# Kernel optimization log

Measured on AMD Instinct MI355X. Metric: run time of the kernel, lower is better.

The kernel has to match this reference:

```python
import jax, jax.numpy as jnp
import numpy as np

B, C, N, M = 4, 192, 160, 160
HEADS, DH = 4, 32
HID = HEADS * DH
NMEM = 4
SCALE = DH ** -0.5


def setup_inputs() -> dict:
    key = jax.random.key(0)
    ks = jax.random.split(key, 8)
    std = 0.05
    return {
        "x": jax.random.normal(ks[0], (B, C, N, M), jnp.float32),
        "gq": jnp.ones((C,), jnp.float32),
        "gk": jnp.ones((C,), jnp.float32),
        "gv": jnp.ones((C,), jnp.float32),
        "Wq": jax.random.normal(ks[1], (HID, C), jnp.float32) * std,
        "Wk": jax.random.normal(ks[2], (HID, C), jnp.float32) * std,
        "Wv": jax.random.normal(ks[3], (HID, C), jnp.float32) * std,
        "mem_kv": jax.random.normal(ks[4], (2, HEADS, NMEM, DH), jnp.float32),
        "Wo": jax.random.normal(ks[5], (C, HID), jnp.float32) * std,
        "bo": jnp.zeros((C,), jnp.float32),
        "Wr": jax.random.normal(ks[6], (C, 2 * C), jnp.float32) * std,
    }


def _rms(x, g):
    # lucidrains RMSNorm over channel axis 1: F.normalize(x, dim=1) * g * sqrt(dim)
    n = jnp.sqrt(jnp.sum(x * x, axis=1, keepdims=True))
    gshape = (1, -1) + (1,) * (x.ndim - 2)
    return x / jnp.maximum(n, 1e-12) * g.reshape(gshape) * jnp.sqrt(jnp.asarray(x.shape[1], x.dtype))


def _axial_attn(q_ft, k_ft, v_map, rep, Wq, Wk, Wv, mem_kv, Wo, bo, gq, gk, gv):
    # q_ft: (b, c, Lq) compact queries (spatial (1,Lq) in the original)
    # k_ft: (b, c, Lk) compact keys; original repeats them `rep` times -> (Lk*rep) keys
    # v_map: (b, c, Lk, rep) values (full map, not broadcast)
    # Exact math of softmax over [NMEM + Lk*rep] keys, exploiting the rep-fold
    # duplicated key scores so attn(key i, copy j) has identical weight p_i:
    #   out = sum_mem p_j mem_v_j + sum_i p_i * (sum_rep v[i, r])
    b = q_ft.shape[0]
    q = jnp.einsum('hdc,bcq->bhqd', Wq.reshape(HEADS, DH, -1), _rms(q_ft, gq))
    k = jnp.einsum('hdc,bck->bhkd', Wk.reshape(HEADS, DH, -1), _rms(k_ft, gk))
    v = jnp.einsum('hdc,bckr->bhkrd', Wv.reshape(HEADS, DH, -1), _rms(v_map, gv))
    v_sum = v.sum(axis=3)  # (b,h,Lk,d)
    mem_k, mem_v = mem_kv[0], mem_kv[1]
    s_k = jnp.einsum('bhqd,bhkd->bhqk', q, k) * SCALE      # (b,h,Lq,Lk)
    s_m = jnp.einsum('bhqd,hjd->bhqj', q, mem_k) * SCALE   # (b,h,Lq,NMEM)
    mx = jnp.maximum(s_k.max(-1), s_m.max(-1))             # (b,h,Lq)
    e_k = jnp.exp(s_k - mx[..., None])
    e_m = jnp.exp(s_m - mx[..., None])
    Z = e_m.sum(-1) + rep * e_k.sum(-1)                    # rep copies of each key
    out = (jnp.einsum('bhqj,hjd->bhqd', e_m, mem_v)
           + jnp.einsum('bhqk,bhkd->bhqd', e_k, v_sum)) / Z[..., None]
    out = out.transpose(0, 2, 1, 3).reshape(b, -1, HID)    # (b,Lq,hid), (h d) channel order
    return jnp.einsum('ck,bqk->bcq', Wo, out) + bo[None, :, None]  # (b,c,Lq)


def reference(x, gq, gk, gv, Wq, Wk, Wv, mem_kv, Wo, bo, Wr):
    # x: (b,c,n,m); mask=None path
    row_ft = x.mean(axis=3)  # (b,c,n)
    col_ft = x.mean(axis=2)  # (b,c,m)
    # row attention: n queries, keys = col_ft repeated n times, values = x^T (spatial (m,n))
    row_attn = _axial_attn(row_ft, col_ft, x.transpose(0, 1, 3, 2), N,
                           Wq, Wk, Wv, mem_kv, Wo, bo, gq, gk, gv)  # (b,c,n)
    # col attention (shared weights): m queries, keys = row_ft repeated m times, values = x
    col_attn = _axial_attn(col_ft, row_ft, x, M,
                           Wq, Wk, Wv, mem_kv, Wo, bo, gq, gk, gv)  # (b,c,m)
    # broadcast to (b,c,n,m), concat on channels, 1x1 conv reduce (bias=False)
    Wr1, Wr2 = Wr[:, :C], Wr[:, C:]
    out = (jnp.einsum('dc,bcn->bdn', Wr1, row_attn)[:, :, :, None]
           + jnp.einsum('dc,bcm->bdm', Wr2, col_attn)[:, :, None, :])
    return out
```

## Files before the change

kernel.cpp:

```cpp
#include <hip/hip_runtime.h>
#include <math.h>

constexpr int B_ = 4, C_ = 192, N_ = 160, M_ = 160;
constexpr int NM_ = N_ * M_;
constexpr float SQRT_C = 13.856406460551018f;
constexpr float SCALE_ = 0.17677669529663687f;

__device__ __forceinline__ float wred_sum(float v) {
    #pragma unroll
    for (int o = 32; o > 0; o >>= 1) v += __shfl_xor(v, o, 64);
    return v;
}
__device__ __forceinline__ float wred_max(float v) {
    #pragma unroll
    for (int o = 32; o > 0; o >>= 1) v = fmaxf(v, __shfl_xor(v, o, 64));
    return v;
}

__global__ void prep_kernel(const float* __restrict__ Wr, const float* __restrict__ Wo,
                            const float* __restrict__ bo,
                            const float* __restrict__ Wq, const float* __restrict__ Wk,
                            const float* __restrict__ Wv, const float* __restrict__ gq,
                            const float* __restrict__ gk, const float* __restrict__ gv,
                            float* __restrict__ WfT, float* __restrict__ bfb,
                            float* __restrict__ WT) {
    int bx = blockIdx.x, tid = threadIdx.x;
    if (bx < 192) {
        int sub = tid >> 7, hd = tid & 127;
        int pair = bx * 2 + sub;
        int t = pair / 192, dch = pair % 192;
        const float* wr = Wr + dch * 384 + t * 192;
        float acc = 0.f;
        for (int c = 0; c < 192; c++) acc += wr[c] * Wo[c * 128 + hd];
        WfT[hd * 384 + pair] = acc;
        if (hd == 0) {
            float s = 0.f;
            for (int c = 0; c < 192; c++) s += wr[c] * bo[c];
            bfb[pair] = s;
        }
    } else {
        int g = (bx - 192) * 256 + tid;
        int mat = g / 24576, r2 = g % 24576;
        int c = r2 >> 7, hd = r2 & 127;
        const float* W = (mat == 0) ? Wq : ((mat == 1) ? Wk : Wv);
        const float* gv_ = (mat == 0) ? gq : ((mat == 1) ? gk : gv);
        WT[g] = gv_[c] * W[hd * 192 + c];
    }
}

__global__ void ssq_part_kernel(const float* __restrict__ x, float* __restrict__ psum) {
    int bx = blockIdx.x;
    int chunk = bx / 400, blk = bx % 400;
    int g = blk * 256 + threadIdx.x;
    int b = g / NM_, nm = g - b * NM_;
    const float* xp = x + ((size_t)(b * C_ + chunk * 32)) * NM_ + nm;
    float ssq = 0.f;
    #pragma unroll
    for (int cc = 0; cc < 32; cc++) { float v = xp[(size_t)cc * NM_]; ssq += v * v; }
    psum[chunk * (B_ * NM_) + g] = ssq;
}

__global__ void rnorm_kernel(const float* __restrict__ psum, float* __restrict__ rn) {
    int g = blockIdx.x * 256 + threadIdx.x;
    float s = 0.f;
    #pragma unroll
    for (int ch = 0; ch < 6; ch++) s += psum[ch * (B_ * NM_) + g];
    rn[g] = SQRT_C / fmaxf(sqrtf(s), 1e-12f);
}

__global__ void rowcol_kernel(const float* __restrict__ x, const float* __restrict__ rn,
                              float* __restrict__ rowft, float* __restrict__ colft,
                              float* __restrict__ Srow, float* __restrict__ Scol) {
    __shared__ float cpart[8][2][160];
    int bc = blockIdx.x;
    int b = bc / C_;
    int tid = threadIdx.x, w = tid >> 6, lane = tid & 63;
    const float* xp = x + (size_t)bc * NM_;
    const float* rp = rn + (size_t)b * NM_;
    int m0 = lane, m1 = lane + 64, m2 = lane + 128;
    bool ok2 = (m2 < M_);
    float cr0 = 0, cr1 = 0, cr2 = 0, cn0 = 0, cn1 = 0, cn2 = 0;
    for (int n = w; n < N_; n += 8) {
        const float* xr = xp + n * M_;
        const float* rr = rp + n * M_;
        float a0 = xr[m0], a1 = xr[m1], a2 = ok2 ? xr[m2] : 0.f;
        float r0 = rr[m0], r1 = rr[m1], r2 = ok2 ? rr[m2] : 0.f;
        float b0 = a0 * r0, b1 = a1 * r1, b2 = a2 * r2;
        cr0 += a0; cr1 += a1; cr2 += a2;
        cn0 += b0; cn1 += b1; cn2 += b2;
        float rs = wred_sum(a0 + a1 + a2);
        float rsn = wred_sum(b0 + b1 + b2);
        if (lane == 0) {
            rowft[bc * N_ + n] = rs * (1.0f / 160.0f);
            Srow[bc * N_ + n] = rsn;
        }
    }
    cpart[w][0][m0] = cr0; cpart[w][0][m1] = cr1; if (ok2) cpart[w][0][m2] = cr2;
    cpart[w][1][m0] = cn0; cpart[w][1][m1] = cn1; if (ok2) cpart[w][1][m2] = cn2;
    __syncthreads();
    if (tid < M_) {
        float sr = 0.f, sn = 0.f;
        #pragma unroll
        for (int ww = 0; ww < 8; ww++) { sr += cpart[ww][0][tid]; sn += cpart[ww][1][tid]; }
        colft[bc * M_ + tid] = sr * (1.0f / 160.0f);
        Scol[bc * M_ + tid] = sn;
    }
}

__global__ void proj_kernel(const float* __restrict__ WT,
                            const float* __restrict__ rowft, const float* __restrict__ colft,
                            const float* __restrict__ Srow, const float* __restrict__ Scol,
                            float* __restrict__ Qb, float* __restrict__ Kb, float* __restrict__ Vb) {
    __shared__ float in_s[192 * 4];
    __shared__ float sc_s[4];
    int bx = blockIdx.x;
    int pt = bx % 40, rest = bx / 40;
    int mat = rest % 3; int r2 = rest / 3;
    int t = r2 % 2, b = r2 / 2;
    const float* src; float* dst;
    if (mat == 0)      { src = (t == 0) ? rowft : colft; dst = Qb; }
    else if (mat == 1) { src = (t == 0) ? colft : rowft; dst = Kb; }
    else               { src = (t == 0) ? Scol  : Srow;  dst = Vb; }
    const float* Wt = WT + mat * 24576;
    int tid = threadIdx.x;
    for (int idx = tid; idx < 192 * 4; idx += 256) {
        int c = idx >> 2, p = idx & 3;
        in_s[idx] = src[(b * C_ + c) * 160 + pt * 4 + p];
    }
    __syncthreads();
    int w = tid >> 6, lane = tid & 63;
    if (mat < 2) {
        float v0 = in_s[lane * 4 + w];
        float v1 = in_s[(lane + 64) * 4 + w];
        float v2 = in_s[(lane + 128) * 4 + w];
        float ssq = wred_sum(v0 * v0 + v1 * v1 + v2 * v2);
        if (lane == 0) sc_s[w] = SQRT_C / fmaxf(sqrtf(ssq), 1e-12f);
    } else {
        if (tid < 4) sc_s[tid] = 1.0f;
    }
    __syncthreads();
    int hd = tid & 127, pc = tid >> 7, p0 = pc * 2;
    float a0 = 0.f, a1 = 0.f;
    for (int c = 0; c < 192; c++) {
        float wv = Wt[c * 128 + hd];
        a0 += wv * in_s[c * 4 + p0];
        a1 += wv * in_s[c * 4 + p0 + 1];
    }
    int posbase = (b * 2 + t) * 160 + pt * 4 + p0;
    dst[(size_t)posbase * 128 + hd]       = a0 * sc_s[p0];
    dst[(size_t)(posbase + 1) * 128 + hd] = a1 * sc_s[p0 + 1];
}

__global__ void attn_kernel(const float* __restrict__ Qb, const float* __restrict__ Kb,
                            const float* __restrict__ Vb, const float* __restrict__ memkv,
                            float* __restrict__ AO) {
    __shared__ float k_s[160 * 33];
    __shared__ float v_s[160 * 33];
    __shared__ float q_s[8 * 33];
    __shared__ float e_s[8 * 160];
    __shared__ float mk[128];
    __shared__ float mv[128];
    int bx = blockIdx.x;
    int qt = bx % 20; int r = bx / 20;
    int h = r & 3; r >>= 2;
    int t = r & 1; int b = r >> 1;
    int tid = threadIdx.x, w = tid >> 6, lane = tid & 63;
    int btbase = ((b * 2 + t) * 160) * 128 + h * 32;
    for (int idx = tid; idx < 160 * 32; idx += 256) {
        int kk = idx >> 5, d = idx & 31;
        k_s[kk * 33 + d] = Kb[btbase + kk * 128 + d];
        v_s[kk * 33 + d] = Vb[btbase + kk * 128 + d];
    }
    { int q = tid >> 5, d = tid & 31;
      q_s[q * 33 + d] = Qb[btbase + (qt * 8 + q) * 128 + d]; }
    if (tid < 128) {
        mk[tid] = memkv[h * 128 + tid];
        mv[tid] = memkv[512 + h * 128 + tid];
    }
    __syncthreads();
    float kr0[32], kr1[32], kr2[32];
    #pragma unroll
    for (int d = 0; d < 32; d++) {
        kr0[d] = k_s[lane * 33 + d];
        kr1[d] = k_s[(lane + 64) * 33 + d];
        kr2[d] = (lane < 32) ? k_s[(lane + 128) * 33 + d] : 0.f;
    }
    float p;
    {
        int pj = lane >> 3, qi = pj >> 2, j = pj & 3;
        int db = (lane & 7) * 4;
        p = 0.f;
        #pragma unroll
        for (int dd = 0; dd < 4; dd++)
            p += q_s[(w * 2 + qi) * 33 + db + dd] * mk[j * 32 + db + dd];
        p += __shfl_xor(p, 1, 64); p += __shfl_xor(p, 2, 64); p += __shfl_xor(p, 4, 64);
        p *= SCALE_;
    }
    float sm[2][4];
    #pragma unroll
    for (int j = 0; j < 4; j++) {
        sm[0][j] = __shfl(p, j * 8, 64);
        sm[1][j] = __shfl(p, 32 + j * 8, 64);
    }
    int dpv = lane & 31;
    float Zq[2], accm[2];
    #pragma unroll
    for (int qi = 0; qi < 2; qi++) {
        int qrow = (w * 2 + qi) * 33;
        float s0 = 0, s1 = 0, s2 = 0;
        #pragma unroll
        for (int d = 0; d < 32; d++) {
            float qv = q_s[qrow + d];
            s0 += qv * kr0[d]; s1 += qv * kr1[d]; s2 += qv * kr2[d];
        }
        s0 *= SCALE_; s1 *= SCALE_;
        s2 = (lane < 32) ? s2 * SCALE_ : -1e30f;
        float mx = fmaxf(fmaxf(s0, s1), s2);
        mx = fmaxf(mx, fmaxf(fmaxf(sm[qi][0], sm[qi][1]), fmaxf(sm[qi][2], sm[qi][3])));
        mx = wred_max(mx);
        float e0 = __expf(s0 - mx), e1 = __expf(s1 - mx);
        float e2 = (lane < 32) ? __expf(s2 - mx) : 0.f;
        int eb = (w * 2 + qi) * 160;
        e_s[eb + lane] = e0; e_s[eb + 64 + lane] = e1;
        if (lane < 32) e_s[eb + 128 + lane] = e2;
        float esum = wred_sum(e0 + e1 + e2);
        float em0 = __expf(sm[qi][0] - mx), em1 = __expf(sm[qi][1] - mx);
        float em2 = __expf(sm[qi][2] - mx), em3 = __expf(sm[qi][3] - mx);
        Zq[qi] = (em0 + em1 + em2 + em3) + 160.0f * esum;
        accm[qi] = em0 * mv[dpv] + em1 * mv[32 + dpv] + em2 * mv[64 + dpv] + em3 * mv[96 + dpv];
    }
    int half = lane >> 5, k0 = half * 80;
    int eb0 = (w * 2) * 160, eb1 = (w * 2 + 1) * 160;
    float a0 = 0, a1 = 0;
    for (int kk = 0; kk < 80; kk++) {
        float v = v_s[(k0 + kk) * 33 + dpv];
        a0 += e_s[eb0 + k0 + kk] * v;
        a1 += e_s[eb1 + k0 + kk] * v;
    }
    a0 += __shfl_down(a0, 32, 64);
    a1 += __shfl_down(a1, 32, 64);
    if (lane < 32) {
        AO[btbase + (qt * 8 + w * 2 + 0) * 128 + lane] = (accm[0] + a0) / Zq[0];
        AO[btbase + (qt * 8 + w * 2 + 1) * 128 + lane] = (accm[1] + a1) / Zq[1];
    }
}

__global__ void oproj_kernel(const float* __restrict__ WfT, const float* __restrict__ bfb,
                             const float* __restrict__ AO, float* __restrict__ Rr,
                             float* __restrict__ Ccv) {
    __shared__ float ao_s[2 * 128];
    int bx = blockIdx.x;
    int pt = bx % 80, rest = bx / 80;
    int t = rest & 1, b = rest >> 1;
    int tid = threadIdx.x;
    for (int idx = tid; idx < 256; idx += 192)
        ao_s[idx] = AO[(size_t)((b * 2 + t) * 160 + pt * 2 + (idx >> 7)) * 128 + (idx & 127)];
    __syncthreads();
    int dch = tid;
    int tofs = t * 192 + dch;
    float a0 = 0.f, a1 = 0.f;
    for (int hd = 0; hd < 128; hd++) {
        float wv = WfT[hd * 384 + tofs];
        a0 += wv * ao_s[hd];
        a1 += wv * ao_s[128 + hd];
    }
    float bb = bfb[tofs];
    float* dst = t ? Ccv : Rr;
    dst[(b * C_ + dch) * 160 + pt * 2 + 0] = a0 + bb;
    dst[(b * C_ + dch) * 160 + pt * 2 + 1] = a1 + bb;
}

__global__ void final_kernel(const float* __restrict__ Rr, const float* __restrict__ Ccv,
                             float* __restrict__ out) {
    __shared__ float Rl[160];
    __shared__ float Cl[160];
    int bd = blockIdx.x;
    int tid = threadIdx.x;
    if (tid < 160) { Rl[tid] = Rr[bd * 160 + tid]; Cl[tid] = Ccv[bd * 160 + tid]; }
    __syncthreads();
    float* base = out + (size_t)bd * NM_;
    for (int idx = tid; idx < 160 * 40; idx += 256) {
        int n = idx / 40, m4 = idx - n * 40;
        float r = Rl[n];
        float4 v;
        v.x = r + Cl[m4 * 4 + 0];
        v.y = r + Cl[m4 * 4 + 1];
        v.z = r + Cl[m4 * 4 + 2];
        v.w = r + Cl[m4 * 4 + 3];
        *reinterpret_cast<float4*>(base + n * 160 + m4 * 4) = v;
    }
}

extern "C" void kernel_launch(void* const* d_in, const int* in_sizes, int n_in,
                              void* d_out, int out_size, void* d_ws, size_t ws_size,
                              hipStream_t stream) {
    const float* x    = (const float*)d_in[0];
    const float* gq   = (const float*)d_in[1];
    const float* gk   = (const float*)d_in[2];
    const float* gv   = (const float*)d_in[3];
    const float* Wq   = (const float*)d_in[4];
    const float* Wk   = (const float*)d_in[5];
    const float* Wv   = (const float*)d_in[6];
    const float* mkv  = (const float*)d_in[7];
    const float* Wo   = (const float*)d_in[8];
    const float* bo   = (const float*)d_in[9];
    const float* Wr   = (const float*)d_in[10];
    float* out = (float*)d_out;

    float* ws = (float*)d_ws;
    float* rn    = ws;
    float* rowft = rn    + 102400;
    float* colft = rowft + 122880;
    float* Srow  = colft + 122880;
    float* Scol  = Srow  + 122880;
    float* WT    = Scol  + 122880;
    float* Qb    = WT    + 73728;
    float* Kb    = Qb    + 163840;
    float* Vb    = Kb    + 163840;
    float* AO    = Vb    + 163840;
    float* Rr    = AO    + 163840;
    float* Ccv   = Rr    + 122880;
    float* WfT   = Ccv   + 122880;
    float* bfb   = WfT   + 49152;
    float* psum  = Qb;

    prep_kernel<<<480, 256, 0, stream>>>(Wr, Wo, bo, Wq, Wk, Wv, gq, gk, gv, WfT, bfb, WT);
    ssq_part_kernel<<<2400, 256, 0, stream>>>(x, psum);
    rnorm_kernel<<<400, 256, 0, stream>>>(psum, rn);
    rowcol_kernel<<<768, 512, 0, stream>>>(x, rn, rowft, colft, Srow, Scol);
    proj_kernel<<<960, 256, 0, stream>>>(WT, rowft, colft, Srow, Scol, Qb, Kb, Vb);
    attn_kernel<<<640, 256, 0, stream>>>(Qb, Kb, Vb, mkv, AO);
    oproj_kernel<<<640, 192, 0, stream>>>(WfT, bfb, AO, Rr, Ccv);
    final_kernel<<<768, 256, 0, stream>>>(Rr, Ccv, out);
}
```

Measured before the change: 226.6 us.

## Fuse norm into prep, fuse oproj with broadcast output, widen proj tiles

Merges the two-stage sum-of-squares reduction into the weight prep kernel: one thread now covers all 192 channels, so the partial-sum buffer goes away. Fuses the output projection into the final broadcast kernel by storing attention output transposed, so each output channel block computes its row and column vectors in place. Doubles the positions per projection block, with float4 shared-memory reads. The main cost targeted is launch count and intermediate round trips; the risks are fewer, longer-running blocks in the norm pass and the projection being recomputed per output block.

```diff
diff --git a/kernel.cpp b/kernel.cpp
--- a/kernel.cpp
+++ b/kernel.cpp
@@ -17,17 +17,26 @@
     return v;
 }
 
-__global__ void prep_kernel(const float* __restrict__ Wr, const float* __restrict__ Wo,
-                            const float* __restrict__ bo,
-                            const float* __restrict__ Wq, const float* __restrict__ Wk,
-                            const float* __restrict__ Wv, const float* __restrict__ gq,
-                            const float* __restrict__ gk, const float* __restrict__ gv,
-                            float* __restrict__ WfT, float* __restrict__ bfb,
-                            float* __restrict__ WT) {
+__global__ void norm_prep_kernel(const float* __restrict__ x,
+                                 const float* __restrict__ Wr, const float* __restrict__ Wo,
+                                 const float* __restrict__ bo,
+                                 const float* __restrict__ Wq, const float* __restrict__ Wk,
+                                 const float* __restrict__ Wv, const float* __restrict__ gq,
+                                 const float* __restrict__ gk, const float* __restrict__ gv,
+                                 float* __restrict__ rn, float* __restrict__ WfT,
+                                 float* __restrict__ bfb, float* __restrict__ WT) {
     int bx = blockIdx.x, tid = threadIdx.x;
-    if (bx < 192) {
+    if (bx < 400) {
+        int g = bx * 256 + tid;
+        int b = g / NM_, nm = g - b * NM_;
+        const float* xp = x + (size_t)b * C_ * NM_ + nm;
+        float ssq = 0.f;
+        #pragma unroll 16
+        for (int c = 0; c < C_; c++) { float v = xp[(size_t)c * NM_]; ssq += v * v; }
+        rn[g] = SQRT_C / fmaxf(sqrtf(ssq), 1e-12f);
+    } else if (bx < 592) {
         int sub = tid >> 7, hd = tid & 127;
-        int pair = bx * 2 + sub;
+        int pair = (bx - 400) * 2 + sub;
         int t = pair / 192, dch = pair % 192;
         const float* wr = Wr + dch * 384 + t * 192;
         float acc = 0.f;
@@ -39,33 +48,13 @@
             bfb[pair] = s;
         }
     } else {
-        int g = (bx - 192) * 256 + tid;
+        int g = (bx - 592) * 256 + tid;
         int mat = g / 24576, r2 = g % 24576;
         int c = r2 >> 7, hd = r2 & 127;
         const float* W = (mat == 0) ? Wq : ((mat == 1) ? Wk : Wv);
-        const float* gv_ = (mat == 0) ? gq : ((mat == 1) ? gk : gv);
-        WT[g] = gv_[c] * W[hd * 192 + c];
-    }
-}
-
-__global__ void ssq_part_kernel(const float* __restrict__ x, float* __restrict__ psum) {
-    int bx = blockIdx.x;
-    int chunk = bx / 400, blk = bx % 400;
-    int g = blk * 256 + threadIdx.x;
-    int b = g / NM_, nm = g - b * NM_;
-    const float* xp = x + ((size_t)(b * C_ + chunk * 32)) * NM_ + nm;
-    float ssq = 0.f;
-    #pragma unroll
-    for (int cc = 0; cc < 32; cc++) { float v = xp[(size_t)cc * NM_]; ssq += v * v; }
-    psum[chunk * (B_ * NM_) + g] = ssq;
-}
-
-__global__ void rnorm_kernel(const float* __restrict__ psum, float* __restrict__ rn) {
-    int g = blockIdx.x * 256 + threadIdx.x;
-    float s = 0.f;
-    #pragma unroll
-    for (int ch = 0; ch < 6; ch++) s += psum[ch * (B_ * NM_) + g];
-    rn[g] = SQRT_C / fmaxf(sqrtf(s), 1e-12f);
+        const float* gg = (mat == 0) ? gq : ((mat == 1) ? gk : gv);
+        WT[g] = gg[c] * W[hd * 192 + c];
+    }
 }
 
 __global__ void rowcol_kernel(const float* __restrict__ x, const float* __restrict__ rn,
@@ -111,10 +100,10 @@
                             const float* __restrict__ rowft, const float* __restrict__ colft,
                             const float* __restrict__ Srow, const float* __restrict__ Scol,
                             float* __restrict__ Qb, float* __restrict__ Kb, float* __restrict__ Vb) {
-    __shared__ float in_s[192 * 4];
-    __shared__ float sc_s[4];
+    __shared__ float in_s[8 * 200];
+    __shared__ float sc_s[8];
     int bx = blockIdx.x;
-    int pt = bx % 40, rest = bx / 40;
+    int pt = bx % 20, rest = bx / 20;
     int mat = rest % 3; int r2 = rest / 3;
     int t = r2 % 2, b = r2 / 2;
     const float* src; float* dst;
@@ -123,37 +112,52 @@
     else               { src = (t == 0) ? Scol  : Srow;  dst = Vb; }
     const float* Wt = WT + mat * 24576;
     int tid = threadIdx.x;
-    for (int idx = tid; idx < 192 * 4; idx += 256) {
-        int c = idx >> 2, p = idx & 3;
-        in_s[idx] = src[(b * C_ + c) * 160 + pt * 4 + p];
+    for (int idx = tid; idx < 192 * 8; idx += 256) {
+        int c = idx >> 3, p = idx & 7;
+        in_s[p * 200 + c] = src[(b * C_ + c) * 160 + pt * 8 + p];
     }
     __syncthreads();
     int w = tid >> 6, lane = tid & 63;
     if (mat < 2) {
-        float v0 = in_s[lane * 4 + w];
-        float v1 = in_s[(lane + 64) * 4 + w];
-        float v2 = in_s[(lane + 128) * 4 + w];
-        float ssq = wred_sum(v0 * v0 + v1 * v1 + v2 * v2);
-        if (lane == 0) sc_s[w] = SQRT_C / fmaxf(sqrtf(ssq), 1e-12f);
+        #pragma unroll
+        for (int qi = 0; qi < 2; qi++) {
+            int pos = w * 2 + qi;
+            float v0 = in_s[pos * 200 + lane];
+            float v1 = in_s[pos * 200 + lane + 64];
+            float v2 = in_s[pos * 200 + lane + 128];
+            float ssq = wred_sum(v0 * v0 + v1 * v1 + v2 * v2);
+            if (lane == 0) sc_s[pos] = SQRT_C / fmaxf(sqrtf(ssq), 1e-12f);
+        }
     } else {
-        if (tid < 4) sc_s[tid] = 1.0f;
-    }
-    __syncthreads();
-    int hd = tid & 127, pc = tid >> 7, p0 = pc * 2;
-    float a0 = 0.f, a1 = 0.f;
-    for (int c = 0; c < 192; c++) {
-        float wv = Wt[c * 128 + hd];
-        a0 += wv * in_s[c * 4 + p0];
-        a1 += wv * in_s[c * 4 + p0 + 1];
-    }
-    int posbase = (b * 2 + t) * 160 + pt * 4 + p0;
-    dst[(size_t)posbase * 128 + hd]       = a0 * sc_s[p0];
+        if (tid < 8) sc_s[tid] = 1.0f;
+    }
+    __syncthreads();
+    int hd = tid & 127, pc = tid >> 7, p0 = pc * 4;
+    float a0 = 0.f, a1 = 0.f, a2 = 0.f, a3 = 0.f;
+    for (int c = 0; c < 192; c += 4) {
+        float w0 = Wt[(c + 0) * 128 + hd];
+        float w1 = Wt[(c + 1) * 128 + hd];
+        float w2 = Wt[(c + 2) * 128 + hd];
+        float w3 = Wt[(c + 3) * 128 + hd];
+        float4 i0 = *reinterpret_cast<const float4*>(&in_s[(p0 + 0) * 200 + c]);
+        float4 i1 = *reinterpret_cast<const float4*>(&in_s[(p0 + 1) * 200 + c]);
+        float4 i2 = *reinterpret_cast<const float4*>(&in_s[(p0 + 2) * 200 + c]);
+        float4 i3 = *reinterpret_cast<const float4*>(&in_s[(p0 + 3) * 200 + c]);
+        a0 += w0 * i0.x + w1 * i0.y + w2 * i0.z + w3 * i0.w;
+        a1 += w0 * i1.x + w1 * i1.y + w2 * i1.z + w3 * i1.w;
+        a2 += w0 * i2.x + w1 * i2.y + w2 * i2.z + w3 * i2.w;
+        a3 += w0 * i3.x + w1 * i3.y + w2 * i3.z + w3 * i3.w;
+    }
+    int posbase = (b * 2 + t) * 160 + pt * 8 + p0;
+    dst[(size_t)(posbase + 0) * 128 + hd] = a0 * sc_s[p0 + 0];
     dst[(size_t)(posbase + 1) * 128 + hd] = a1 * sc_s[p0 + 1];
+    dst[(size_t)(posbase + 2) * 128 + hd] = a2 * sc_s[p0 + 2];
+    dst[(size_t)(posbase + 3) * 128 + hd] = a3 * sc_s[p0 + 3];
 }
 
 __global__ void attn_kernel(const float* __restrict__ Qb, const float* __restrict__ Kb,
                             const float* __restrict__ Vb, const float* __restrict__ memkv,
-                            float* __restrict__ AO) {
+                            float* __restrict__ AOT) {
     __shared__ float k_s[160 * 33];
     __shared__ float v_s[160 * 33];
     __shared__ float q_s[8 * 33];
@@ -240,46 +244,34 @@
     a0 += __shfl_down(a0, 32, 64);
     a1 += __shfl_down(a1, 32, 64);
     if (lane < 32) {
-        AO[btbase + (qt * 8 + w * 2 + 0) * 128 + lane] = (accm[0] + a0) / Zq[0];
-        AO[btbase + (qt * 8 + w * 2 + 1) * 128 + lane] = (accm[1] + a1) / Zq[1];
-    }
-}
-
-__global__ void oproj_kernel(const float* __restrict__ WfT, const float* __restrict__ bfb,
-                             const float* __restrict__ AO, float* __restrict__ Rr,
-                             float* __restrict__ Ccv) {
-    __shared__ float ao_s[2 * 128];
-    int bx = blockIdx.x;
-    int pt = bx % 80, rest = bx / 80;
-    int t = rest & 1, b = rest >> 1;
-    int tid = threadIdx.x;
-    for (int idx = tid; idx < 256; idx += 192)
-        ao_s[idx] = AO[(size_t)((b * 2 + t) * 160 + pt * 2 + (idx >> 7)) * 128 + (idx & 127)];
-    __syncthreads();
-    int dch = tid;
-    int tofs = t * 192 + dch;
-    float a0 = 0.f, a1 = 0.f;
-    for (int hd = 0; hd < 128; hd++) {
-        float wv = WfT[hd * 384 + tofs];
-        a0 += wv * ao_s[hd];
-        a1 += wv * ao_s[128 + hd];
-    }
-    float bb = bfb[tofs];
-    float* dst = t ? Ccv : Rr;
-    dst[(b * C_ + dch) * 160 + pt * 2 + 0] = a0 + bb;
-    dst[(b * C_ + dch) * 160 + pt * 2 + 1] = a1 + bb;
-}
-
-__global__ void final_kernel(const float* __restrict__ Rr, const float* __restrict__ Ccv,
-                             float* __restrict__ out) {
+        int aobase = (b * 2 + t) * 20480 + (h * 32 + lane) * 160 + qt * 8 + w * 2;
+        AOT[aobase + 0] = (accm[0] + a0) / Zq[0];
+        AOT[aobase + 1] = (accm[1] + a1) / Zq[1];
+    }
+}
+
+__global__ void oproj_final_kernel(const float* __restrict__ WfT, const float* __restrict__ bfb,
+                                   const float* __restrict__ AOT, float* __restrict__ out) {
     __shared__ float Rl[160];
     __shared__ float Cl[160];
-    int bd = blockIdx.x;
+    int bx = blockIdx.x;
+    int b = bx / C_, dch = bx % C_;
     int tid = threadIdx.x;
-    if (tid < 160) { Rl[tid] = Rr[bd * 160 + tid]; Cl[tid] = Ccv[bd * 160 + tid]; }
-    __syncthreads();
-    float* base = out + (size_t)bd * NM_;
-    for (int idx = tid; idx < 160 * 40; idx += 256) {
+    if (tid < 320) {
+        int t = (tid >= 160) ? 1 : 0;
+        int p = t ? (tid - 160) : tid;
+        const float* ao = AOT + (b * 2 + t) * 20480 + p;
+        const float* wf = WfT + t * 192 + dch;
+        float acc = 0.f;
+        #pragma unroll 8
+        for (int hd = 0; hd < 128; hd++)
+            acc += wf[hd * 384] * ao[hd * 160];
+        acc += bfb[t * 192 + dch];
+        if (t) Cl[p] = acc; else Rl[p] = acc;
+    }
+    __syncthreads();
+    float* base = out + (size_t)bx * NM_;
+    for (int idx = tid; idx < 160 * 40; idx += 320) {
         int n = idx / 40, m4 = idx - n * 40;
         float r = Rl[n];
         float4 v;
@@ -317,19 +309,14 @@
     float* Qb    = WT    + 73728;
     float* Kb    = Qb    + 163840;
     float* Vb    = Kb    + 163840;
-    float* AO    = Vb    + 163840;
-    float* Rr    = AO    + 163840;
-    float* Ccv   = Rr    + 122880;
-    float* WfT   = Ccv   + 122880;
+    float* AOT   = Vb    + 163840;
+    float* WfT   = AOT   + 163840;
     float* bfb   = WfT   + 49152;
-    float* psum  = Qb;
-
-    prep_kernel<<<480, 256, 0, stream>>>(Wr, Wo, bo, Wq, Wk, Wv, gq, gk, gv, WfT, bfb, WT);
-    ssq_part_kernel<<<2400, 256, 0, stream>>>(x, psum);
-    rnorm_kernel<<<400, 256, 0, stream>>>(psum, rn);
+
+    norm_prep_kernel<<<880, 256, 0, stream>>>(x, Wr, Wo, bo, Wq, Wk, Wv, gq, gk, gv,
+                                              rn, WfT, bfb, WT);
     rowcol_kernel<<<768, 512, 0, stream>>>(x, rn, rowft, colft, Srow, Scol);
-    proj_kernel<<<960, 256, 0, stream>>>(WT, rowft, colft, Srow, Scol, Qb, Kb, Vb);
-    attn_kernel<<<640, 256, 0, stream>>>(Qb, Kb, Vb, mkv, AO);
-    oproj_kernel<<<640, 192, 0, stream>>>(WfT, bfb, AO, Rr, Ccv);
-    final_kernel<<<768, 256, 0, stream>>>(Rr, Ccv, out);
-}
+    proj_kernel<<<480, 256, 0, stream>>>(WT, rowft, colft, Srow, Scol, Qb, Kb, Vb);
+    attn_kernel<<<640, 256, 0, stream>>>(Qb, Kb, Vb, mkv, AOT);
+    oproj_final_kernel<<<768, 320, 0, stream>>>(WfT, bfb, AOT, out);
+}
```

Measured after the change: 229.1 us. No clear change (+1.1%).
